# Performance work log

Hardware: AMD Instinct MI355X
Metric: run time of the kernel (lower is better)

The kernel has to match this reference:

```python
import jax, jax.numpy as jnp
import numpy as np

COEFF = 0.97  # de-emphasis coefficient (module init kwarg)


def setup_inputs() -> dict:
    key = jax.random.key(0)
    waveform = jax.random.normal(key, (32, 2, 480000), dtype=jnp.float32)
    return {"waveform": waveform}


def reference(waveform) -> jnp.ndarray:
    # y[n] = x[n] + COEFF * y[n-1] along the last axis.
    # Expressed as a first-order linear recurrence y_n = a_n*y_{n-1} + b_n
    # with a_n = COEFF (constant), b_n = x[n], solved with a log-depth
    # associative scan: (a1,b1) o (a2,b2) = (a1*a2, a2*b1 + b2).
    a = jnp.full_like(waveform, COEFF)

    def combine(left, right):
        a_l, b_l = left
        a_r, b_r = right
        return (a_l * a_r, a_r * b_l + b_r)

    _, y = jax.lax.associative_scan(combine, (a, waveform), axis=-1)
    return y
```

## Files before the change

kernel.cpp:

```cpp
#include <hip/hip_runtime.h>


#define COEFF 0.97f
#define ROW_LEN 480000
#define SPAN_W 256
#define HALO 512
#define P_HALO 2
#define P_OUT 15
#define P_TOT (P_OUT + P_HALO)
#define OUT_W (P_OUT * SPAN_W)
#define WPR (ROW_LEN / OUT_W)
#define BLOCK 256
#define WAVES (BLOCK / 64)

typedef float v4f __attribute__((ext_vector_type(4)));

constexpr float fpow(float b, int n) {
    float r = 1.0f;
    for (int i = 0; i < n; ++i) r *= b;
    return r;
}
constexpr float S0 = fpow(COEFF, 4);
constexpr float S1 = fpow(COEFF, 8);
constexpr float S2 = fpow(COEFF, 16);
constexpr float S3 = fpow(COEFF, 32);
constexpr float S4 = fpow(COEFF, 64);
constexpr float S5 = fpow(COEFF, 128);
constexpr float CP  = fpow(COEFF, SPAN_W);
constexpr float C1P = fpow(COEFF, 1);
constexpr float C2P = fpow(COEFF, 2);
constexpr float C3P = fpow(COEFF, 3);
constexpr float C4P = fpow(COEFF, 4);
constexpr float IC4 = 1.0f / fpow(COEFF, 4);

__device__ __forceinline__ float bcast63(float v) {
    return __int_as_float(__builtin_amdgcn_readlane(__float_as_int(v), 63));
}

__global__ __launch_bounds__(BLOCK, 8) void deemph_kernel(const float* __restrict__ x,
                                                          float* __restrict__ y,
                                                          int n_rows) {
    const int lane = threadIdx.x & 63;
    const int wave = threadIdx.x >> 6;
    const int gw   = blockIdx.x * WAVES + wave;
    const int row  = gw / WPR;
    const int widx = gw - row * WPR;
    if (row >= n_rows) return;

    const float* __restrict__ xrow = x + (long long)row * ROW_LEN;
    float* __restrict__ yrow       = y + (long long)row * ROW_LEN;

    const int lbase = widx * OUT_W - HALO + 4 * lane;
    const bool row_start = (widx == 0);

    float Aex = 1.0f;
    if (lane & 1)  Aex *= S0;
    if (lane & 2)  Aex *= S1;
    if (lane & 4)  Aex *= S2;
    if (lane & 8)  Aex *= S3;
    if (lane & 16) Aex *= S4;
    if (lane & 32) Aex *= S5;

    float c = 0.0f;
    #pragma unroll
    for (int p = 0; p < P_TOT; ++p) {
        int e = lbase + p * SPAN_W;
        const int ec = e < 0 ? 0 : e;
        const v4f v = __builtin_nontemporal_load((const v4f*)(xrow + ec));

        const float l0 = v.x;
        const float l1 = fmaf(COEFF, l0, v.y);
        const float l2 = fmaf(COEFF, l1, v.z);
        const float l3 = fmaf(COEFF, l2, v.w);

        float Bv = l3, Bp;
        Bp = __shfl_up(Bv, 1);  if (lane >= 1)  Bv = fmaf(S0, Bp, Bv);
        Bp = __shfl_up(Bv, 2);  if (lane >= 2)  Bv = fmaf(S1, Bp, Bv);
        Bp = __shfl_up(Bv, 4);  if (lane >= 4)  Bv = fmaf(S2, Bp, Bv);
        Bp = __shfl_up(Bv, 8);  if (lane >= 8)  Bv = fmaf(S3, Bp, Bv);
        Bp = __shfl_up(Bv, 16); if (lane >= 16) Bv = fmaf(S4, Bp, Bv);
        Bp = __shfl_up(Bv, 32); if (lane >= 32) Bv = fmaf(S5, Bp, Bv);

        const float Bex = (Bv - l3) * IC4;
        const float B63 = bcast63(Bv);

        float cc = c;
        if (p == P_HALO && row_start) cc = 0.0f;
        const float Kt = fmaf(cc, Aex, Bex);
        c = fmaf(cc, CP, B63);

        if (p >= P_HALO) {
            v4f o;
            o.x = fmaf(Kt, C1P, l0);
            o.y = fmaf(Kt, C2P, l1);
            o.z = fmaf(Kt, C3P, l2);
            o.w = fmaf(Kt, C4P, l3);
            __builtin_nontemporal_store(o, (v4f*)(yrow + e));
        }
    }
}

extern "C" void kernel_launch(void* const* d_in, const int* in_sizes, int n_in,
                              void* d_out, int out_size, void* d_ws, size_t ws_size,
                              hipStream_t stream) {
    (void)n_in; (void)d_ws; (void)ws_size; (void)out_size;
    const float* x = (const float*)d_in[0];
    float* y = (float*)d_out;
    const int n_rows = in_sizes[0] / ROW_LEN;
    const int nblocks = (WPR * n_rows + WAVES - 1) / WAVES;
    deemph_kernel<<<dim3(nblocks), BLOCK, 0, stream>>>(x, y, n_rows);
}
```

Before: 209.3 us.

## Process two independent chunks per wave and shrink chunk output width

Each wave now scans two chunks, one from the first half of the work list and one from the second, with their loads, shuffle scans and stores interleaved to raise instruction-level parallelism. The output span per chunk is cut from 15 to 5 strips, which gives more parallel chunks. The cost is a larger share of redundant halo loads per output element and higher register pressure. The split also assumes the total chunk count is even.

```diff
diff --git a/kernel.cpp b/kernel.cpp
--- a/kernel.cpp
+++ b/kernel.cpp
@@ -6,7 +6,7 @@
 #define SPAN_W 256
 #define HALO 512
 #define P_HALO 2
-#define P_OUT 15
+#define P_OUT 5
 #define P_TOT (P_OUT + P_HALO)
 #define OUT_W (P_OUT * SPAN_W)
 #define WPR (ROW_LEN / OUT_W)
@@ -43,15 +43,24 @@
     const int lane = threadIdx.x & 63;
     const int wave = threadIdx.x >> 6;
     const int gw   = blockIdx.x * WAVES + wave;
-    const int row  = gw / WPR;
-    const int widx = gw - row * WPR;
-    if (row >= n_rows) return;
+    const int n_half = (WPR * n_rows) >> 1;
+    if (gw >= n_half) return;
 
-    const float* __restrict__ xrow = x + (long long)row * ROW_LEN;
-    float* __restrict__ yrow       = y + (long long)row * ROW_LEN;
+    const int iA = gw;
+    const int iB = gw + n_half;
 
-    const int lbase = widx * OUT_W - HALO + 4 * lane;
-    const bool row_start = (widx == 0);
+    const int rowA = iA / WPR, widxA = iA - rowA * WPR;
+    const int rowB = iB / WPR, widxB = iB - rowB * WPR;
+
+    const float* __restrict__ xrowA = x + (long long)rowA * ROW_LEN;
+    float* __restrict__ yrowA       = y + (long long)rowA * ROW_LEN;
+    const float* __restrict__ xrowB = x + (long long)rowB * ROW_LEN;
+    float* __restrict__ yrowB       = y + (long long)rowB * ROW_LEN;
+
+    const int lbA = widxA * OUT_W - HALO + 4 * lane;
+    const int lbB = widxB * OUT_W - HALO + 4 * lane;
+    const bool rsA = (widxA == 0);
+    const bool rsB = (widxB == 0);
 
     float Aex = 1.0f;
     if (lane & 1)  Aex *= S0;
@@ -61,41 +70,62 @@
     if (lane & 16) Aex *= S4;
     if (lane & 32) Aex *= S5;
 
-    float c = 0.0f;
+    float cA = 0.0f, cB = 0.0f;
     #pragma unroll
     for (int p = 0; p < P_TOT; ++p) {
-        int e = lbase + p * SPAN_W;
-        const int ec = e < 0 ? 0 : e;
-        const v4f v = __builtin_nontemporal_load((const v4f*)(xrow + ec));
+        const int eA = lbA + p * SPAN_W;
+        const int eB = lbB + p * SPAN_W;
+        const int ecA = eA < 0 ? 0 : eA;
+        const int ecB = eB < 0 ? 0 : eB;
+        const v4f vA = __builtin_nontemporal_load((const v4f*)(xrowA + ecA));
+        const v4f vB = __builtin_nontemporal_load((const v4f*)(xrowB + ecB));
 
-        const float l0 = v.x;
-        const float l1 = fmaf(COEFF, l0, v.y);
-        const float l2 = fmaf(COEFF, l1, v.z);
-        const float l3 = fmaf(COEFF, l2, v.w);
+        const float a0 = vA.x;
+        const float b0 = vB.x;
+        const float a1 = fmaf(COEFF, a0, vA.y);
+        const float b1 = fmaf(COEFF, b0, vB.y);
+        const float a2 = fmaf(COEFF, a1, vA.z);
+        const float b2 = fmaf(COEFF, b1, vB.z);
+        const float a3 = fmaf(COEFF, a2, vA.w);
+        const float b3 = fmaf(COEFF, b2, vB.w);
 
-        float Bv = l3, Bp;
-        Bp = __shfl_up(Bv, 1);  if (lane >= 1)  Bv = fmaf(S0, Bp, Bv);
-        Bp = __shfl_up(Bv, 2);  if (lane >= 2)  Bv = fmaf(S1, Bp, Bv);
-        Bp = __shfl_up(Bv, 4);  if (lane >= 4)  Bv = fmaf(S2, Bp, Bv);
-        Bp = __shfl_up(Bv, 8);  if (lane >= 8)  Bv = fmaf(S3, Bp, Bv);
-        Bp = __shfl_up(Bv, 16); if (lane >= 16) Bv = fmaf(S4, Bp, Bv);
-        Bp = __shfl_up(Bv, 32); if (lane >= 32) Bv = fmaf(S5, Bp, Bv);
+        float BA = a3, BB = b3, pA, pB;
+        pA = __shfl_up(BA, 1);  pB = __shfl_up(BB, 1);
+        if (lane >= 1)  { BA = fmaf(S0, pA, BA); BB = fmaf(S0, pB, BB); }
+        pA = __shfl_up(BA, 2);  pB = __shfl_up(BB, 2);
+        if (lane >= 2)  { BA = fmaf(S1, pA, BA); BB = fmaf(S1, pB, BB); }
+        pA = __shfl_up(BA, 4);  pB = __shfl_up(BB, 4);
+        if (lane >= 4)  { BA = fmaf(S2, pA, BA); BB = fmaf(S2, pB, BB); }
+        pA = __shfl_up(BA, 8);  pB = __shfl_up(BB, 8);
+        if (lane >= 8)  { BA = fmaf(S3, pA, BA); BB = fmaf(S3, pB, BB); }
+        pA = __shfl_up(BA, 16); pB = __shfl_up(BB, 16);
+        if (lane >= 16) { BA = fmaf(S4, pA, BA); BB = fmaf(S4, pB, BB); }
+        pA = __shfl_up(BA, 32); pB = __shfl_up(BB, 32);
+        if (lane >= 32) { BA = fmaf(S5, pA, BA); BB = fmaf(S5, pB, BB); }
 
-        const float Bex = (Bv - l3) * IC4;
-        const float B63 = bcast63(Bv);
+        const float BexA = (BA - a3) * IC4;
+        const float BexB = (BB - b3) * IC4;
+        const float B63A = bcast63(BA);
+        const float B63B = bcast63(BB);
 
-        float cc = c;
-        if (p == P_HALO && row_start) cc = 0.0f;
-        const float Kt = fmaf(cc, Aex, Bex);
-        c = fmaf(cc, CP, B63);
+        float ccA = cA, ccB = cB;
+        if (p == P_HALO) {
+            if (rsA) ccA = 0.0f;
+            if (rsB) ccB = 0.0f;
+        }
+        const float KtA = fmaf(ccA, Aex, BexA);
+        const float KtB = fmaf(ccB, Aex, BexB);
+        cA = fmaf(ccA, CP, B63A);
+        cB = fmaf(ccB, CP, B63B);
 
         if (p >= P_HALO) {
-            v4f o;
-            o.x = fmaf(Kt, C1P, l0);
-            o.y = fmaf(Kt, C2P, l1);
-            o.z = fmaf(Kt, C3P, l2);
-            o.w = fmaf(Kt, C4P, l3);
-            __builtin_nontemporal_store(o, (v4f*)(yrow + e));
+            v4f oA, oB;
+            oA.x = fmaf(KtA, C1P, a0);  oB.x = fmaf(KtB, C1P, b0);
+            oA.y = fmaf(KtA, C2P, a1);  oB.y = fmaf(KtB, C2P, b1);
+            oA.z = fmaf(KtA, C3P, a2);  oB.z = fmaf(KtB, C3P, b2);
+            oA.w = fmaf(KtA, C4P, a3);  oB.w = fmaf(KtB, C4P, b3);
+            __builtin_nontemporal_store(oA, (v4f*)(yrowA + eA));
+            __builtin_nontemporal_store(oB, (v4f*)(yrowB + eB));
         }
     }
 }
@@ -106,7 +136,8 @@
     (void)n_in; (void)d_ws; (void)ws_size; (void)out_size;
     const float* x = (const float*)d_in[0];
     float* y = (float*)d_out;
-    const int n_rows = in_sizes[0] / ROW_LEN;
-    const int nblocks = (WPR * n_rows + WAVES - 1) / WAVES;
+    const int n_rows  = in_sizes[0] / ROW_LEN;
+    const int n_half  = (WPR * n_rows) / 2;
+    const int nblocks = (n_half + WAVES - 1) / WAVES;
     deemph_kernel<<<dim3(nblocks), BLOCK, 0, stream>>>(x, y, n_rows);
 }
```

After: 207.8 us. About the same (-0.7%).
